# Kernel optimization log

Measured on AMD Instinct MI355X. Metric: run time of the kernel, lower is better.

Reference implementation:

```python
import jax, jax.numpy as jnp
import numpy as np

B, L, H = 32, 2048, 1024


def setup_inputs() -> dict:
    key = jax.random.key(0)
    k1, k2, k3, k4, k5 = jax.random.split(key, 5)
    stdv = 1.0 / np.sqrt(H)
    return {
        "hidden": jax.random.normal(k1, (B, H), dtype=jnp.float32),
        "encoder_outputs": jax.random.normal(k2, (L, B, H), dtype=jnp.float32),
        "attn_w": jax.random.normal(k3, (H, 2 * H), dtype=jnp.float32) * stdv,
        "attn_b": jax.random.normal(k4, (H,), dtype=jnp.float32) * stdv,
        "v": jax.random.normal(k5, (H,), dtype=jnp.float32) * stdv,
    }


def reference(hidden, encoder_outputs, attn_w, attn_b, v):
    # encoder_outputs: [L, B, H] -> batch-first [B, L, H]
    enc = jnp.transpose(encoder_outputs, (1, 0, 2))
    # Additive (Bahdanau) energies. Split the concat-linear into two GEMMs to
    # avoid materializing the [B, L, 2H] concat:
    #   attn([H_rep, enc]) = hidden @ W_h^T + enc @ W_e^T + b
    w_h, w_e = attn_w[:, :H], attn_w[:, H:]  # each [H, 2H]->[H, H]
    proj = (jnp.einsum("bh,oh->bo", hidden, w_h)[:, None, :]
            + jnp.einsum("blh,oh->blo", enc, w_e)
            + attn_b)
    energy = jnp.tanh(proj)                   # [B, L, H]
    scores = jnp.einsum("blh,h->bl", energy, v)  # [B, L]
    attn = jax.nn.softmax(scores, axis=-1)       # [B, L]
    context = jnp.einsum("bl,blh->bh", attn, enc)  # [B, H]
    return context[None, :, :]  # [1, B, H] matching context.transpose(0,1)
```

## Files before the change

kernel.cpp:

```cpp
#include <hip/hip_runtime.h>
#include <hip/hip_bf16.h>
#include <math.h>

#define Hdim 1024
#define Bdim 32
#define Ldim 2048
#define Mtot (Bdim*Ldim)

typedef __attribute__((ext_vector_type(8))) short short8v;
typedef __attribute__((ext_vector_type(4))) short short4v;
typedef __attribute__((ext_vector_type(4))) float floatx4;

static __device__ inline short f2bf(float f) {
    union { float f; unsigned u; } x; x.f = f;
    unsigned r = x.u + 0x7FFF + ((x.u >> 16) & 1);
    return (short)(r >> 16);
}
static __device__ inline float bf2f(short s) {
    union { unsigned u; float f; } x; x.u = ((unsigned)(unsigned short)s) << 16;
    return x.f;
}

static __device__ inline float fast_tanh(float x) {
    float t = 2.0f * x;
    t = fminf(fmaxf(t, -30.0f), 30.0f);
    float e = __expf(t);
    return (e - 1.0f) / (e + 1.0f);
}

typedef __attribute__((address_space(1))) const void GVT;
typedef __attribute__((address_space(3))) void LVT;
static __device__ inline void gload_lds16(const void* g, void* l) {
    __builtin_amdgcn_global_load_lds((GVT*)g, (LVT*)l, 16, 0, 0);
}

__global__ __launch_bounds__(256) void convert_enc_kernel(
    const float* __restrict__ enc, short* __restrict__ enc_bf)
{
    size_t i = ((size_t)blockIdx.x * 256 + threadIdx.x) * 8;
    float4 a = *(const float4*)(enc + i);
    float4 b = *(const float4*)(enc + i + 4);
    short8v o;
    o[0]=f2bf(a.x); o[1]=f2bf(a.y); o[2]=f2bf(a.z); o[3]=f2bf(a.w);
    o[4]=f2bf(b.x); o[5]=f2bf(b.y); o[6]=f2bf(b.z); o[7]=f2bf(b.w);
    *(short8v*)(enc_bf + i) = o;
}

__global__ __launch_bounds__(256) void convert_w_kernel(
    const float* __restrict__ attn_w, short* __restrict__ w_bf)
{
    int t = blockIdx.x * 256 + threadIdx.x;
    int o = t >> 7;
    int c = t & 127;
    const float* src = attn_w + (size_t)o * 2 * Hdim + Hdim + c * 8;
    float4 a = *(const float4*)(src);
    float4 b = *(const float4*)(src + 4);
    short8v v;
    v[0]=f2bf(a.x); v[1]=f2bf(a.y); v[2]=f2bf(a.z); v[3]=f2bf(a.w);
    v[4]=f2bf(b.x); v[5]=f2bf(b.y); v[6]=f2bf(b.z); v[7]=f2bf(b.w);
    *(short8v*)(w_bf + (size_t)o * Hdim + c * 8) = v;
}

__global__ __launch_bounds__(256) void qproj_kernel(
    const float* __restrict__ hidden, const float* __restrict__ attn_w,
    const float* __restrict__ attn_b, float* __restrict__ qbuf)
{
    int w = blockIdx.x * 4 + (threadIdx.x >> 6);
    int lane = threadIdx.x & 63;
    int o = w >> 5;
    int b = w & 31;
    const float* hrow = hidden + b * Hdim;
    const float* wrow = attn_w + (size_t)o * 2 * Hdim;
    float s = 0.f;
    #pragma unroll
    for (int i = 0; i < 16; i++) s += hrow[lane + i*64] * wrow[lane + i*64];
    s += __shfl_xor(s, 1);  s += __shfl_xor(s, 2);  s += __shfl_xor(s, 4);
    s += __shfl_xor(s, 8);  s += __shfl_xor(s, 16); s += __shfl_xor(s, 32);
    if (lane == 0) qbuf[b * Hdim + o] = s + attn_b[o];
}

#define NKT 16

__global__ __launch_bounds__(512, 1) void scores_kernel(
    const short* __restrict__ enc_bf,
    const short* __restrict__ w_bf,
    const float* __restrict__ qbuf,
    const float* __restrict__ vvec,
    float* __restrict__ spart)
{
    __shared__ short As[2][256*64];
    __shared__ short Bs[2][256*64];
    __shared__ float sred[256][4];

    int hw  = blockIdx.x;
    int xcd = hw & 7;
    int i7  = hw >> 3;
    int nblk  = i7 & 3;
    int mtile = xcd * 32 + (i7 >> 2);
    int m0 = mtile * 256;
    int n0 = nblk * 256;

    int tid = threadIdx.x;
    int w   = tid >> 6;
    int l   = tid & 63;
    int wr  = w >> 2;
    int wc  = w & 3;
    int r15 = l & 15;
    int kc  = l >> 4;
    int rg  = l >> 4;

    const int glsw = (l >> 3) * Hdim + (((l & 7) ^ (l >> 3)) * 8);

#define STAGE_A(h, bb, k0) do { \
    const short* _g = enc_bf + (size_t)(m0 + (h)*128 + w*16) * Hdim + (k0) + glsw; \
    gload_lds16(_g,            &As[bb][(h)*8192 + w*1024]);        \
    gload_lds16(_g + 8*Hdim,   &As[bb][(h)*8192 + w*1024 + 512]);  \
} while (0)
#define STAGE_B(h, bb, k0) do { \
    const short* _g = w_bf + (size_t)(n0 + (h)*128 + w*16) * Hdim + (k0) + glsw; \
    gload_lds16(_g,            &Bs[bb][(h)*8192 + w*1024]);        \
    gload_lds16(_g + 8*Hdim,   &Bs[bb][(h)*8192 + w*1024 + 512]);  \
} while (0)
#define LDA(mi, kk) (*(const short8v*)(&As[cur][(wr*128 + (mi)*16 + r15)*64 + ((((kk)*4 + kc) ^ (l & 7)) * 8)]))
#define LDB(ni, kk) (*(const short8v*)(&Bs[cur][(wc*64  + (ni)*16 + r15)*64 + ((((kk)*4 + kc) ^ (l & 7)) * 8)]))

    floatx4 acc[8][4];
    #pragma unroll
    for (int i = 0; i < 8; i++)
        #pragma unroll
        for (int j = 0; j < 4; j++) acc[i][j] = (floatx4){0.f, 0.f, 0.f, 0.f};

    short8v af[4][2], bf[4][2];

    STAGE_A(0, 0, 0); STAGE_A(1, 0, 0);
    STAGE_B(0, 0, 0); STAGE_B(1, 0, 0);
    asm volatile("s_waitcnt vmcnt(0)" ::: "memory");
    __syncthreads();

    for (int kt = 0; kt < NKT; kt++) {
        int cur = kt & 1;
        int nxt = cur ^ 1;
        int kn  = (kt + 1) * 64;
        bool pf = (kt < NKT - 1);

        #pragma unroll
        for (int mi = 0; mi < 4; mi++)
            #pragma unroll
            for (int kk = 0; kk < 2; kk++) af[mi][kk] = LDA(mi, kk);
        #pragma unroll
        for (int ni = 0; ni < 2; ni++)
            #pragma unroll
            for (int kk = 0; kk < 2; kk++) bf[ni][kk] = LDB(ni, kk);
        if (pf) { STAGE_A(0, nxt, kn); STAGE_A(1, nxt, kn); }
        __builtin_amdgcn_s_barrier();
        __builtin_amdgcn_s_setprio(1);
        #pragma unroll
        for (int mi = 0; mi < 4; mi++)
            #pragma unroll
            for (int ni = 0; ni < 2; ni++)
                #pragma unroll
                for (int kk = 0; kk < 2; kk++)
                    acc[mi][ni] = __builtin_amdgcn_mfma_f32_16x16x32_bf16(af[mi][kk], bf[ni][kk], acc[mi][ni], 0, 0, 0);
        __builtin_amdgcn_s_setprio(0);
        __builtin_amdgcn_s_barrier();

        #pragma unroll
        for (int ni = 2; ni < 4; ni++)
            #pragma unroll
            for (int kk = 0; kk < 2; kk++) bf[ni][kk] = LDB(ni, kk);
        if (pf) { STAGE_B(0, nxt, kn); STAGE_B(1, nxt, kn); }
        __builtin_amdgcn_s_barrier();
        __builtin_amdgcn_s_setprio(1);
        #pragma unroll
        for (int mi = 0; mi < 4; mi++)
            #pragma unroll
            for (int ni = 2; ni < 4; ni++)
                #pragma unroll
                for (int kk = 0; kk < 2; kk++)
                    acc[mi][ni] = __builtin_amdgcn_mfma_f32_16x16x32_bf16(af[mi][kk], bf[ni][kk], acc[mi][ni], 0, 0, 0);
        __builtin_amdgcn_s_setprio(0);
        __builtin_amdgcn_s_barrier();

        #pragma unroll
        for (int mi = 0; mi < 4; mi++)
            #pragma unroll
            for (int kk = 0; kk < 2; kk++) af[mi][kk] = LDA(mi + 4, kk);
        __builtin_amdgcn_s_barrier();
        __builtin_amdgcn_s_setprio(1);
        #pragma unroll
        for (int mi = 0; mi < 4; mi++)
            #pragma unroll
            for (int ni = 0; ni < 2; ni++)
                #pragma unroll
                for (int kk = 0; kk < 2; kk++)
                    acc[mi + 4][ni] = __builtin_amdgcn_mfma_f32_16x16x32_bf16(af[mi][kk], bf[ni][kk], acc[mi + 4][ni], 0, 0, 0);
        __builtin_amdgcn_s_setprio(0);
        __builtin_amdgcn_s_barrier();

        if (pf) asm volatile("s_waitcnt vmcnt(0)" ::: "memory");
        __builtin_amdgcn_s_barrier();
        __builtin_amdgcn_s_setprio(1);
        #pragma unroll
        for (int mi = 0; mi < 4; mi++)
            #pragma unroll
            for (int ni = 2; ni < 4; ni++)
                #pragma unroll
                for (int kk = 0; kk < 2; kk++)
                    acc[mi + 4][ni] = __builtin_amdgcn_mfma_f32_16x16x32_bf16(af[mi][kk], bf[ni][kk], acc[mi + 4][ni], 0, 0, 0);
        __builtin_amdgcn_s_setprio(0);
        __builtin_amdgcn_s_barrier();
    }

    #pragma unroll
    for (int mi = 0; mi < 8; mi++) {
        float rs[4] = {0.f, 0.f, 0.f, 0.f};
        #pragma unroll
        for (int ni = 0; ni < 4; ni++) {
            int o = n0 + wc*64 + ni*16 + r15;
            float vo = vvec[o];
            #pragma unroll
            for (int reg = 0; reg < 4; reg++) {
                int r = wr*128 + mi*16 + rg*4 + reg;
                float p = acc[mi][ni][reg] + qbuf[(r & 31) * Hdim + o];
                rs[reg] += fast_tanh(p) * vo;
            }
        }
        #pragma unroll
        for (int reg = 0; reg < 4; reg++) {
            float s = rs[reg];
            s += __shfl_xor(s, 1); s += __shfl_xor(s, 2);
            s += __shfl_xor(s, 4); s += __shfl_xor(s, 8);
            if (r15 == 0) {
                int r = wr*128 + mi*16 + rg*4 + reg;
                sred[r][wc] = s;
            }
        }
    }
    __syncthreads();
    if (tid < 256)
        spart[(size_t)nblk * Mtot + m0 + tid] = sred[tid][0] + sred[tid][1] + sred[tid][2] + sred[tid][3];
#undef STAGE_A
#undef STAGE_B
#undef LDA
#undef LDB
}

__global__ __launch_bounds__(256) void softmax_kernel(
    const float* __restrict__ spart,
    float* __restrict__ attn)
{
    int b = blockIdx.x;
    int t = threadIdx.x;
    __shared__ float rmax[4], rsum[4];
    float sv[8];
    float mx = -1e30f;
    #pragma unroll
    for (int i = 0; i < 8; i++) {
        int l = t + i * 256;
        int m = l * Bdim + b;
        float s = 0.f;
        #pragma unroll
        for (int p = 0; p < 4; p++) s += spart[(size_t)p * Mtot + m];
        sv[i] = s;
        mx = fmaxf(mx, s);
    }
    #pragma unroll
    for (int off = 1; off < 64; off <<= 1) mx = fmaxf(mx, __shfl_xor(mx, off));
    if ((t & 63) == 0) rmax[t >> 6] = mx;
    __syncthreads();
    mx = fmaxf(fmaxf(rmax[0], rmax[1]), fmaxf(rmax[2], rmax[3]));
    float sum = 0.f;
    #pragma unroll
    for (int i = 0; i < 8; i++) { sv[i] = __expf(sv[i] - mx); sum += sv[i]; }
    #pragma unroll
    for (int off = 1; off < 64; off <<= 1) sum += __shfl_xor(sum, off);
    if ((t & 63) == 0) rsum[t >> 6] = sum;
    __syncthreads();
    sum = rsum[0] + rsum[1] + rsum[2] + rsum[3];
    float inv = 1.f / sum;
    #pragma unroll
    for (int i = 0; i < 8; i++)
        attn[(size_t)b * Ldim + t + i * 256] = sv[i] * inv;
}

__global__ __launch_bounds__(256) void context_part_kernel(
    const short* __restrict__ enc_bf,
    const float* __restrict__ attn,
    float* __restrict__ cpart)
{
    int b = blockIdx.x & 31;
    int c = blockIdx.x >> 5;
    int t = threadIdx.x;
    float a0 = 0.f, a1 = 0.f, a2 = 0.f, a3 = 0.f;
    int l0 = c * 32;
    for (int i = 0; i < 32; i++) {
        int l = l0 + i;
        float a = attn[(size_t)b * Ldim + l];
        short4v e = *(const short4v*)(enc_bf + (size_t)(l * Bdim + b) * Hdim + t * 4);
        a0 += a * bf2f(e.x); a1 += a * bf2f(e.y);
        a2 += a * bf2f(e.z); a3 += a * bf2f(e.w);
    }
    float4 r; r.x = a0; r.y = a1; r.z = a2; r.w = a3;
    *(float4*)(cpart + ((size_t)c * Bdim + b) * Hdim + t * 4) = r;
}

__global__ __launch_bounds__(256) void context_reduce_kernel(
    const float* __restrict__ cpart, float* __restrict__ out)
{
    int idx = blockIdx.x * 256 + threadIdx.x;
    float s = 0.f;
    for (int c = 0; c < 64; c++) s += cpart[(size_t)c * (Bdim * Hdim) + idx];
    out[idx] = s;
}

extern "C" void kernel_launch(void* const* d_in, const int* in_sizes, int n_in,
                              void* d_out, int out_size, void* d_ws, size_t ws_size,
                              hipStream_t stream)
{
    const float* hidden = (const float*)d_in[0];
    const float* enc    = (const float*)d_in[1];
    const float* attn_w = (const float*)d_in[2];
    const float* attn_b = (const float*)d_in[3];
    const float* vvec   = (const float*)d_in[4];
    float* out = (float*)d_out;

    char* ws = (char*)d_ws;
    size_t off = 0;
    short* enc_bf = (short*)(ws + off); off += (size_t)Mtot * Hdim * 2;
    short* w_bf   = (short*)(ws + off); off += (size_t)Hdim * Hdim * 2;
    float* qbuf   = (float*)(ws + off); off += (size_t)Bdim * Hdim * 4;
    float* spart  = (float*)(ws + off); off += (size_t)4 * Mtot * 4;
    float* attnp  = (float*)(ws + off); off += (size_t)Mtot * 4;
    float* cpart  = (float*)(ws + off);

    convert_enc_kernel<<<32768, 256, 0, stream>>>(enc, enc_bf);
    convert_w_kernel<<<512, 256, 0, stream>>>(attn_w, w_bf);
    qproj_kernel<<<8192, 256, 0, stream>>>(hidden, attn_w, attn_b, qbuf);
    scores_kernel<<<1024, 512, 0, stream>>>(enc_bf, w_bf, qbuf, vvec, spart);
    softmax_kernel<<<Bdim, 256, 0, stream>>>(spart, attnp);
    context_part_kernel<<<2048, 256, 0, stream>>>(enc_bf, attnp, cpart);
    context_reduce_kernel<<<128, 256, 0, stream>>>(cpart, out);
}
```

Baseline: 285.3 us.

## Switch scores GEMM to triple-buffered K=32 pipeline with one barrier per step

The scores GEMM main loop moves from a double-buffered K=64 tile with four barrier-separated MFMA phases per iteration to a three-stage ring of K=32 tiles. Each step has one wait and one barrier, and loads are issued two steps ahead under partial vmcnt waits. The LDS swizzle is changed to match 32-wide rows. The aim is to hide global-load latency better and cut barrier overhead. In exchange there are twice as many loop iterations and more fragment registers live per step (8 A plus 4 B).

```diff
diff --git a/kernel.cpp b/kernel.cpp
--- a/kernel.cpp
+++ b/kernel.cpp
@@ -79,7 +79,7 @@
     if (lane == 0) qbuf[b * Hdim + o] = s + attn_b[o];
 }
 
-#define NKT 16
+#define NKT 32
 
 __global__ __launch_bounds__(512, 1) void scores_kernel(
     const short* __restrict__ enc_bf,
@@ -88,8 +88,8 @@
     const float* __restrict__ vvec,
     float* __restrict__ spart)
 {
-    __shared__ short As[2][256*64];
-    __shared__ short Bs[2][256*64];
+    __shared__ short As[3][256*32];
+    __shared__ short Bs[3][256*32];
     __shared__ float sred[256][4];
 
     int hw  = blockIdx.x;
@@ -107,22 +107,26 @@
     int wc  = w & 3;
     int r15 = l & 15;
     int kc  = l >> 4;
-    int rg  = l >> 4;
-
-    const int glsw = (l >> 3) * Hdim + (((l & 7) ^ (l >> 3)) * 8);
-
-#define STAGE_A(h, bb, k0) do { \
-    const short* _g = enc_bf + (size_t)(m0 + (h)*128 + w*16) * Hdim + (k0) + glsw; \
-    gload_lds16(_g,            &As[bb][(h)*8192 + w*1024]);        \
-    gload_lds16(_g + 8*Hdim,   &As[bb][(h)*8192 + w*1024 + 512]);  \
+
+    int srow = l >> 2;
+    int ssw  = (srow ^ (srow >> 2)) & 3;
+    const int glsw = srow * Hdim + (((l & 3) ^ ssw) * 8);
+
+#define STAGE_A(bb, k0) do { \
+    const short* _g = enc_bf + (size_t)(m0 + w*16) * Hdim + (k0) + glsw; \
+    gload_lds16(_g,                    &As[bb][(w*16)*32]);       \
+    gload_lds16(_g + (size_t)128*Hdim, &As[bb][(w*16+128)*32]);   \
 } while (0)
-#define STAGE_B(h, bb, k0) do { \
-    const short* _g = w_bf + (size_t)(n0 + (h)*128 + w*16) * Hdim + (k0) + glsw; \
-    gload_lds16(_g,            &Bs[bb][(h)*8192 + w*1024]);        \
-    gload_lds16(_g + 8*Hdim,   &Bs[bb][(h)*8192 + w*1024 + 512]);  \
+#define STAGE_B(bb, k0) do { \
+    const short* _g = w_bf + (size_t)(n0 + w*16) * Hdim + (k0) + glsw; \
+    gload_lds16(_g,                    &Bs[bb][(w*16)*32]);       \
+    gload_lds16(_g + (size_t)128*Hdim, &Bs[bb][(w*16+128)*32]);   \
 } while (0)
-#define LDA(mi, kk) (*(const short8v*)(&As[cur][(wr*128 + (mi)*16 + r15)*64 + ((((kk)*4 + kc) ^ (l & 7)) * 8)]))
-#define LDB(ni, kk) (*(const short8v*)(&Bs[cur][(wc*64  + (ni)*16 + r15)*64 + ((((kk)*4 + kc) ^ (l & 7)) * 8)]))
+
+    int s15 = (r15 ^ (r15 >> 2)) & 3;
+    int rc  = (kc ^ s15) * 8;
+#define LDA(mi) (*(const short8v*)(&As[cur][(wr*128 + (mi)*16 + r15)*32 + rc]))
+#define LDB(ni) (*(const short8v*)(&Bs[cur][(wc*64  + (ni)*16 + r15)*32 + rc]))
 
     floatx4 acc[8][4];
     #pragma unroll
@@ -130,85 +134,36 @@
         #pragma unroll
         for (int j = 0; j < 4; j++) acc[i][j] = (floatx4){0.f, 0.f, 0.f, 0.f};
 
-    short8v af[4][2], bf[4][2];
-
-    STAGE_A(0, 0, 0); STAGE_A(1, 0, 0);
-    STAGE_B(0, 0, 0); STAGE_B(1, 0, 0);
-    asm volatile("s_waitcnt vmcnt(0)" ::: "memory");
-    __syncthreads();
-
-    for (int kt = 0; kt < NKT; kt++) {
-        int cur = kt & 1;
-        int nxt = cur ^ 1;
-        int kn  = (kt + 1) * 64;
-        bool pf = (kt < NKT - 1);
-
-        #pragma unroll
-        for (int mi = 0; mi < 4; mi++)
+    STAGE_A(0, 0);  STAGE_B(0, 0);
+    STAGE_A(1, 32); STAGE_B(1, 32);
+
+    int cur = 0;
+    for (int t = 0; t < NKT; t++) {
+        if (t < NKT - 1) asm volatile("s_waitcnt vmcnt(4)" ::: "memory");
+        else             asm volatile("s_waitcnt vmcnt(0)" ::: "memory");
+        __builtin_amdgcn_s_barrier();
+
+        short8v af[8], bf[4];
+        #pragma unroll
+        for (int mi = 0; mi < 8; mi++) af[mi] = LDA(mi);
+        #pragma unroll
+        for (int ni = 0; ni < 4; ni++) bf[ni] = LDB(ni);
+
+        if (t + 2 < NKT) {
+            int nb = cur + 2; if (nb >= 3) nb -= 3;
+            STAGE_A(nb, (t + 2) * 32);
+            STAGE_B(nb, (t + 2) * 32);
+        }
+
+        __builtin_amdgcn_s_setprio(1);
+        #pragma unroll
+        for (int mi = 0; mi < 8; mi++)
             #pragma unroll
-            for (int kk = 0; kk < 2; kk++) af[mi][kk] = LDA(mi, kk);
-        #pragma unroll
-        for (int ni = 0; ni < 2; ni++)
-            #pragma unroll
-            for (int kk = 0; kk < 2; kk++) bf[ni][kk] = LDB(ni, kk);
-        if (pf) { STAGE_A(0, nxt, kn); STAGE_A(1, nxt, kn); }
-        __builtin_amdgcn_s_barrier();
-        __builtin_amdgcn_s_setprio(1);
-        #pragma unroll
-        for (int mi = 0; mi < 4; mi++)
-            #pragma unroll
-            for (int ni = 0; ni < 2; ni++)
-                #pragma unroll
-                for (int kk = 0; kk < 2; kk++)
-                    acc[mi][ni] = __builtin_amdgcn_mfma_f32_16x16x32_bf16(af[mi][kk], bf[ni][kk], acc[mi][ni], 0, 0, 0);
+            for (int ni = 0; ni < 4; ni++)
+                acc[mi][ni] = __builtin_amdgcn_mfma_f32_16x16x32_bf16(af[mi], bf[ni], acc[mi][ni], 0, 0, 0);
         __builtin_amdgcn_s_setprio(0);
-        __builtin_amdgcn_s_barrier();
-
-        #pragma unroll
-        for (int ni = 2; ni < 4; ni++)
-            #pragma unroll
-            for (int kk = 0; kk < 2; kk++) bf[ni][kk] = LDB(ni, kk);
-        if (pf) { STAGE_B(0, nxt, kn); STAGE_B(1, nxt, kn); }
-        __builtin_amdgcn_s_barrier();
-        __builtin_amdgcn_s_setprio(1);
-        #pragma unroll
-        for (int mi = 0; mi < 4; mi++)
-            #pragma unroll
-            for (int ni = 2; ni < 4; ni++)
-                #pragma unroll
-                for (int kk = 0; kk < 2; kk++)
-                    acc[mi][ni] = __builtin_amdgcn_mfma_f32_16x16x32_bf16(af[mi][kk], bf[ni][kk], acc[mi][ni], 0, 0, 0);
-        __builtin_amdgcn_s_setprio(0);
-        __builtin_amdgcn_s_barrier();
-
-        #pragma unroll
-        for (int mi = 0; mi < 4; mi++)
-            #pragma unroll
-            for (int kk = 0; kk < 2; kk++) af[mi][kk] = LDA(mi + 4, kk);
-        __builtin_amdgcn_s_barrier();
-        __builtin_amdgcn_s_setprio(1);
-        #pragma unroll
-        for (int mi = 0; mi < 4; mi++)
-            #pragma unroll
-            for (int ni = 0; ni < 2; ni++)
-                #pragma unroll
-                for (int kk = 0; kk < 2; kk++)
-                    acc[mi + 4][ni] = __builtin_amdgcn_mfma_f32_16x16x32_bf16(af[mi][kk], bf[ni][kk], acc[mi + 4][ni], 0, 0, 0);
-        __builtin_amdgcn_s_setprio(0);
-        __builtin_amdgcn_s_barrier();
-
-        if (pf) asm volatile("s_waitcnt vmcnt(0)" ::: "memory");
-        __builtin_amdgcn_s_barrier();
-        __builtin_amdgcn_s_setprio(1);
-        #pragma unroll
-        for (int mi = 0; mi < 4; mi++)
-            #pragma unroll
-            for (int ni = 2; ni < 4; ni++)
-                #pragma unroll
-                for (int kk = 0; kk < 2; kk++)
-                    acc[mi + 4][ni] = __builtin_amdgcn_mfma_f32_16x16x32_bf16(af[mi][kk], bf[ni][kk], acc[mi + 4][ni], 0, 0, 0);
-        __builtin_amdgcn_s_setprio(0);
-        __builtin_amdgcn_s_barrier();
+
+        cur++; if (cur >= 3) cur -= 3;
     }
 
     #pragma unroll
@@ -220,7 +175,7 @@
             float vo = vvec[o];
             #pragma unroll
             for (int reg = 0; reg < 4; reg++) {
-                int r = wr*128 + mi*16 + rg*4 + reg;
+                int r = wr*128 + mi*16 + kc*4 + reg;
                 float p = acc[mi][ni][reg] + qbuf[(r & 31) * Hdim + o];
                 rs[reg] += fast_tanh(p) * vo;
             }
@@ -231,7 +186,7 @@
             s += __shfl_xor(s, 1); s += __shfl_xor(s, 2);
             s += __shfl_xor(s, 4); s += __shfl_xor(s, 8);
             if (r15 == 0) {
-                int r = wr*128 + mi*16 + rg*4 + reg;
+                int r = wr*128 + mi*16 + kc*4 + reg;
                 sred[r][wc] = s;
             }
         }
```

Result: no change. 283.4 us (-0.7%).

## Split GEMM tile into four quadrants with staggered half-tile prefetch waits

Applied to the files above, without the earlier changes.

Restructures the scores GEMM main loop so each warp computes four 64x32 sub-tiles (one per half of A and half of B), and global-to-LDS prefetch is issued per half-tile with partial vmcnt waits instead of a full drain each iteration. The warp-to-tile mapping and LDS swizzle pattern change, and the epilogue is adapted to the new quadrant accumulators. The goal is to overlap the next tile's loads with MFMA work more finely and to reduce LDS bank conflicts, at the risk of subtle vmcnt accounting or synchronization errors.

```diff
diff --git a/kernel.cpp b/kernel.cpp
--- a/kernel.cpp
+++ b/kernel.cpp
@@ -88,8 +88,8 @@
     const float* __restrict__ vvec,
     float* __restrict__ spart)
 {
-    __shared__ short As[2][256*64];
-    __shared__ short Bs[2][256*64];
+    __shared__ short As[2][2][8192];
+    __shared__ short Bs[2][2][8192];
     __shared__ float sred[256][4];
 
     int hw  = blockIdx.x;
@@ -109,49 +109,60 @@
     int kc  = l >> 4;
     int rg  = l >> 4;
 
-    const int glsw = (l >> 3) * Hdim + (((l & 7) ^ (l >> 3)) * 8);
+    int lrow = l >> 3;
+    int lch  = l & 7;
+    int swz0 = ((l >> 5) << 1) & 7;
+    int swz1 = (4 + ((l >> 5) << 1)) & 7;
+    const int gl0 = lrow * Hdim + ((lch ^ swz0) * 8);
+    const int gl1 = lrow * Hdim + ((lch ^ swz1) * 8);
 
 #define STAGE_A(h, bb, k0) do { \
-    const short* _g = enc_bf + (size_t)(m0 + (h)*128 + w*16) * Hdim + (k0) + glsw; \
-    gload_lds16(_g,            &As[bb][(h)*8192 + w*1024]);        \
-    gload_lds16(_g + 8*Hdim,   &As[bb][(h)*8192 + w*1024 + 512]);  \
+    const short* _g = enc_bf + (size_t)(m0 + (h)*128 + w*16) * Hdim + (k0); \
+    gload_lds16(_g + gl0,                      &As[bb][h][w*1024]);       \
+    gload_lds16(_g + 8*(size_t)Hdim + gl1,     &As[bb][h][w*1024 + 512]); \
 } while (0)
 #define STAGE_B(h, bb, k0) do { \
-    const short* _g = w_bf + (size_t)(n0 + (h)*128 + w*16) * Hdim + (k0) + glsw; \
-    gload_lds16(_g,            &Bs[bb][(h)*8192 + w*1024]);        \
-    gload_lds16(_g + 8*Hdim,   &Bs[bb][(h)*8192 + w*1024 + 512]);  \
+    const short* _g = w_bf + (size_t)(n0 + (h)*128 + w*16) * Hdim + (k0); \
+    gload_lds16(_g + gl0,                      &Bs[bb][h][w*1024]);       \
+    gload_lds16(_g + 8*(size_t)Hdim + gl1,     &Bs[bb][h][w*1024 + 512]); \
 } while (0)
-#define LDA(mi, kk) (*(const short8v*)(&As[cur][(wr*128 + (mi)*16 + r15)*64 + ((((kk)*4 + kc) ^ (l & 7)) * 8)]))
-#define LDB(ni, kk) (*(const short8v*)(&Bs[cur][(wc*64  + (ni)*16 + r15)*64 + ((((kk)*4 + kc) ^ (l & 7)) * 8)]))
-
-    floatx4 acc[8][4];
-    #pragma unroll
-    for (int i = 0; i < 8; i++)
-        #pragma unroll
-        for (int j = 0; j < 4; j++) acc[i][j] = (floatx4){0.f, 0.f, 0.f, 0.f};
-
-    short8v af[4][2], bf[4][2];
-
-    STAGE_A(0, 0, 0); STAGE_A(1, 0, 0);
-    STAGE_B(0, 0, 0); STAGE_B(1, 0, 0);
-    asm volatile("s_waitcnt vmcnt(0)" ::: "memory");
-    __syncthreads();
-
-    for (int kt = 0; kt < NKT; kt++) {
-        int cur = kt & 1;
+
+    int q2 = (r15 >> 2) * 2;
+#define LDA(h, mi, kk) (*(const short8v*)(&As[cur][h][(wr*64 + (mi)*16 + r15)*64 + ((((kk)*4 + kc) ^ q2) * 8)]))
+#define LDB(h, ni, kk) (*(const short8v*)(&Bs[cur][h][(wc*32 + (ni)*16 + r15)*64 + ((((kk)*4 + kc) ^ q2) * 8)]))
+
+    floatx4 accA[4][2], accB[4][2], accC[4][2], accD[4][2];
+    #pragma unroll
+    for (int i = 0; i < 4; i++)
+        #pragma unroll
+        for (int j = 0; j < 2; j++) {
+            accA[i][j] = (floatx4){0.f,0.f,0.f,0.f};
+            accB[i][j] = (floatx4){0.f,0.f,0.f,0.f};
+            accC[i][j] = (floatx4){0.f,0.f,0.f,0.f};
+            accD[i][j] = (floatx4){0.f,0.f,0.f,0.f};
+        }
+
+    short8v af[4][2], bf0[2][2], bf1[2][2];
+
+    STAGE_A(0, 0, 0); STAGE_B(0, 0, 0); STAGE_B(1, 0, 0); STAGE_A(1, 0, 0);
+    asm volatile("s_waitcnt vmcnt(4)" ::: "memory");
+    __builtin_amdgcn_s_barrier();
+
+    for (int t = 0; t < NKT; t++) {
+        int cur = t & 1;
         int nxt = cur ^ 1;
-        int kn  = (kt + 1) * 64;
-        bool pf = (kt < NKT - 1);
-
-        #pragma unroll
-        for (int mi = 0; mi < 4; mi++)
-            #pragma unroll
-            for (int kk = 0; kk < 2; kk++) af[mi][kk] = LDA(mi, kk);
+        int kn  = (t + 1) * 64;
+        bool pf = (t < NKT - 1);
+
+        #pragma unroll
+        for (int mi = 0; mi < 4; mi++)
+            #pragma unroll
+            for (int kk = 0; kk < 2; kk++) af[mi][kk] = LDA(0, mi, kk);
         #pragma unroll
         for (int ni = 0; ni < 2; ni++)
             #pragma unroll
-            for (int kk = 0; kk < 2; kk++) bf[ni][kk] = LDB(ni, kk);
-        if (pf) { STAGE_A(0, nxt, kn); STAGE_A(1, nxt, kn); }
+            for (int kk = 0; kk < 2; kk++) bf0[ni][kk] = LDB(0, ni, kk);
+        if (pf) STAGE_A(0, nxt, kn);
         __builtin_amdgcn_s_barrier();
         __builtin_amdgcn_s_setprio(1);
         #pragma unroll
@@ -160,31 +171,36 @@
             for (int ni = 0; ni < 2; ni++)
                 #pragma unroll
                 for (int kk = 0; kk < 2; kk++)
-                    acc[mi][ni] = __builtin_amdgcn_mfma_f32_16x16x32_bf16(af[mi][kk], bf[ni][kk], acc[mi][ni], 0, 0, 0);
+                    accA[mi][ni] = __builtin_amdgcn_mfma_f32_16x16x32_bf16(af[mi][kk], bf0[ni][kk], accA[mi][ni], 0, 0, 0);
         __builtin_amdgcn_s_setprio(0);
-        __builtin_amdgcn_s_barrier();
-
-        #pragma unroll
-        for (int ni = 2; ni < 4; ni++)
-            #pragma unroll
-            for (int kk = 0; kk < 2; kk++) bf[ni][kk] = LDB(ni, kk);
-        if (pf) { STAGE_B(0, nxt, kn); STAGE_B(1, nxt, kn); }
+        if (pf) asm volatile("s_waitcnt vmcnt(4)" ::: "memory");
+        else    asm volatile("s_waitcnt vmcnt(2)" ::: "memory");
+        __builtin_amdgcn_s_barrier();
+
+        #pragma unroll
+        for (int ni = 0; ni < 2; ni++)
+            #pragma unroll
+            for (int kk = 0; kk < 2; kk++) bf1[ni][kk] = LDB(1, ni, kk);
+        if (pf) STAGE_B(0, nxt, kn);
         __builtin_amdgcn_s_barrier();
         __builtin_amdgcn_s_setprio(1);
         #pragma unroll
         for (int mi = 0; mi < 4; mi++)
             #pragma unroll
-            for (int ni = 2; ni < 4; ni++)
+            for (int ni = 0; ni < 2; ni++)
                 #pragma unroll
                 for (int kk = 0; kk < 2; kk++)
-                    acc[mi][ni] = __builtin_amdgcn_mfma_f32_16x16x32_bf16(af[mi][kk], bf[ni][kk], acc[mi][ni], 0, 0, 0);
+                    accB[mi][ni] = __builtin_amdgcn_mfma_f32_16x16x32_bf16(af[mi][kk], bf1[ni][kk], accB[mi][ni], 0, 0, 0);
         __builtin_amdgcn_s_setprio(0);
-        __builtin_amdgcn_s_barrier();
-
-        #pragma unroll
-        for (int mi = 0; mi < 4; mi++)
-            #pragma unroll
-            for (int kk = 0; kk < 2; kk++) af[mi][kk] = LDA(mi + 4, kk);
+        if (pf) asm volatile("s_waitcnt vmcnt(4)" ::: "memory");
+        else    asm volatile("s_waitcnt vmcnt(0)" ::: "memory");
+        __builtin_amdgcn_s_barrier();
+
+        #pragma unroll
+        for (int mi = 0; mi < 4; mi++)
+            #pragma unroll
+            for (int kk = 0; kk < 2; kk++) af[mi][kk] = LDA(1, mi, kk);
+        if (pf) STAGE_B(1, nxt, kn);
         __builtin_amdgcn_s_barrier();
         __builtin_amdgcn_s_setprio(1);
         #pragma unroll
@@ -193,49 +209,56 @@
             for (int ni = 0; ni < 2; ni++)
                 #pragma unroll
                 for (int kk = 0; kk < 2; kk++)
-                    acc[mi + 4][ni] = __builtin_amdgcn_mfma_f32_16x16x32_bf16(af[mi][kk], bf[ni][kk], acc[mi + 4][ni], 0, 0, 0);
+                    accC[mi][ni] = __builtin_amdgcn_mfma_f32_16x16x32_bf16(af[mi][kk], bf0[ni][kk], accC[mi][ni], 0, 0, 0);
         __builtin_amdgcn_s_setprio(0);
         __builtin_amdgcn_s_barrier();
 
-        if (pf) asm volatile("s_waitcnt vmcnt(0)" ::: "memory");
+        if (pf) STAGE_A(1, nxt, kn);
         __builtin_amdgcn_s_barrier();
         __builtin_amdgcn_s_setprio(1);
         #pragma unroll
         for (int mi = 0; mi < 4; mi++)
             #pragma unroll
-            for (int ni = 2; ni < 4; ni++)
+            for (int ni = 0; ni < 2; ni++)
                 #pragma unroll
                 for (int kk = 0; kk < 2; kk++)
-                    acc[mi + 4][ni] = __builtin_amdgcn_mfma_f32_16x16x32_bf16(af[mi][kk], bf[ni][kk], acc[mi + 4][ni], 0, 0, 0);
+                    accD[mi][ni] = __builtin_amdgcn_mfma_f32_16x16x32_bf16(af[mi][kk], bf1[ni][kk], accD[mi][ni], 0, 0, 0);
         __builtin_amdgcn_s_setprio(0);
+        if (pf) asm volatile("s_waitcnt vmcnt(4)" ::: "memory");
         __builtin_amdgcn_s_barrier();
     }
 
     #pragma unroll
-    for (int mi = 0; mi < 8; mi++) {
-        float rs[4] = {0.f, 0.f, 0.f, 0.f};
-        #pragma unroll
-        for (int ni = 0; ni < 4; ni++) {
-            int o = n0 + wc*64 + ni*16 + r15;
-            float vo = vvec[o];
+    for (int qm = 0; qm < 2; qm++)
+        #pragma unroll
+        for (int mi = 0; mi < 4; mi++) {
+            float rs[4] = {0.f, 0.f, 0.f, 0.f};
+            #pragma unroll
+            for (int ni = 0; ni < 2; ni++) {
+                floatx4 f0 = qm ? accC[mi][ni] : accA[mi][ni];
+                floatx4 f1 = qm ? accD[mi][ni] : accB[mi][ni];
+                int o0 = n0 + wc*32 + ni*16 + r15;
+                int o1 = o0 + 128;
+                float v0 = vvec[o0], v1 = vvec[o1];
+                #pragma unroll
+                for (int reg = 0; reg < 4; reg++) {
+                    int r = qm*128 + wr*64 + mi*16 + rg*4 + reg;
+                    int b = r & 31;
+                    rs[reg] += fast_tanh(f0[reg] + qbuf[b * Hdim + o0]) * v0;
+                    rs[reg] += fast_tanh(f1[reg] + qbuf[b * Hdim + o1]) * v1;
+                }
+            }
             #pragma unroll
             for (int reg = 0; reg < 4; reg++) {
-                int r = wr*128 + mi*16 + rg*4 + reg;
-                float p = acc[mi][ni][reg] + qbuf[(r & 31) * Hdim + o];
-                rs[reg] += fast_tanh(p) * vo;
+                float s = rs[reg];
+                s += __shfl_xor(s, 1); s += __shfl_xor(s, 2);
+                s += __shfl_xor(s, 4); s += __shfl_xor(s, 8);
+                if (r15 == 0) {
+                    int r = qm*128 + wr*64 + mi*16 + rg*4 + reg;
+                    sred[r][wc] = s;
+                }
             }
         }
-        #pragma unroll
-        for (int reg = 0; reg < 4; reg++) {
-            float s = rs[reg];
-            s += __shfl_xor(s, 1); s += __shfl_xor(s, 2);
-            s += __shfl_xor(s, 4); s += __shfl_xor(s, 8);
-            if (r15 == 0) {
-                int r = wr*128 + mi*16 + rg*4 + reg;
-                sred[r][wc] = s;
-            }
-        }
-    }
     __syncthreads();
     if (tid < 256)
         spart[(size_t)nblk * Mtot + m0 + tid] = sred[tid][0] + sred[tid][1] + sred[tid][2] + sred[tid][3];
```

Measured after the change: 302.9 us. +6.2%, slower.
